# Kernel optimization log

Measured on AMD Instinct MI355X. Metric: run time of the kernel, lower is better.

## Reference

```python
import jax, jax.numpy as jnp
import numpy as np

N = 100000      # nodes
E = 1600000     # edges (before self loops)
F_IN = 256      # num_features
HID = 8         # hid per head, layer 1
H1 = 8          # in_head
H2 = 4          # out_head
NCLS = 40       # num_classes


def setup_inputs() -> dict:
    key = jax.random.key(0)
    ks = jax.random.split(key, 10)
    p = lambda k, shape: jax.random.normal(k, shape, jnp.float32) * 0.1
    d1 = H1 * HID   # 64
    d2 = H2 * NCLS  # 160
    return dict(
        x=jax.random.normal(ks[0], (N, F_IN), jnp.float32),
        edge_index=jax.random.randint(ks[1], (2, E), 0, N),
        Wl1=p(ks[2], (F_IN, d1)), bl1=jnp.zeros((d1,), jnp.float32),
        Wr1=p(ks[3], (F_IN, d1)), br1=jnp.zeros((d1,), jnp.float32),
        att1=p(ks[4], (H1, HID)), b1=jnp.zeros((d1,), jnp.float32),
        Wl2=p(ks[5], (d1, d2)), bl2=jnp.zeros((d2,), jnp.float32),
        Wr2=p(ks[6], (d1, d2)), br2=jnp.zeros((d2,), jnp.float32),
        att2=p(ks[7], (H2, NCLS)), b2=jnp.zeros((NCLS,), jnp.float32),
    )


def gatv2_conv(x, src, dst, Wl, bl, Wr, br, att, bias, heads, ch, concat):
    """PyG GATv2Conv (eval mode): lin_l -> source/messages, lin_r -> target."""
    n = x.shape[0]
    xl = (x @ Wl + bl).reshape(n, heads, ch)   # source-side features
    xr = (x @ Wr + br).reshape(n, heads, ch)   # target-side features
    # edge-wise attention logits: LeakyReLU(x_i + x_j) . att
    e = jax.nn.leaky_relu(xl[src] + xr[dst], 0.2)          # [E, H, C]
    logits = jnp.einsum('ehc,hc->eh', e, att)               # [E, H]
    # segment softmax over incoming edges of each destination node
    m = jax.ops.segment_max(logits, dst, num_segments=n)    # [N, H]
    ex = jnp.exp(logits - m[dst])
    s = jax.ops.segment_sum(ex, dst, num_segments=n)        # [N, H]
    alpha = ex / (s[dst] + 1e-16)                           # [E, H]
    # scatter-add weighted source messages
    out = jax.ops.segment_sum(xl[src] * alpha[:, :, None], dst, num_segments=n)  # [N, H, C]
    if concat:
        return out.reshape(n, heads * ch) + bias
    return out.mean(axis=1) + bias


def reference(x, edge_index, Wl1, bl1, Wr1, br1, att1, b1,
              Wl2, bl2, Wr2, br2, att2, b2):
    n = x.shape[0]
    loop = jnp.arange(n)
    # PyG GATv2Conv default add_self_loops=True
    src = jnp.concatenate([edge_index[0], loop])
    dst = jnp.concatenate([edge_index[1], loop])
    # eval mode: all dropout (input, inter-layer, attention) disabled
    h = gatv2_conv(x, src, dst, Wl1, bl1, Wr1, br1, att1, b1, H1, HID, True)
    h = jax.nn.elu(h)
    out = gatv2_conv(h, src, dst, Wl2, bl2, Wr2, br2, att2, b2, H2, NCLS, False)
    return jax.nn.log_softmax(out, axis=1)
```

## Files before the change

kernel.cpp:

```cpp
#include <hip/hip_runtime.h>
#include <math.h>

#define NN 100000
#define EE 1600000
#define FIN 256
#define D1 64
#define D2 160
#define C2 40
#define PK1 264
#define PK2 72
#define NBUCK 391
#define CAP 5000
#define WSCL 0.015625f
#define L2E 1.442695041f

typedef unsigned short u16;
typedef __attribute__((ext_vector_type(8))) short bf16x8;
typedef __attribute__((ext_vector_type(4))) float f32x4;
typedef _Float16 h2t __attribute__((ext_vector_type(2)));
union hu { unsigned u; h2t h; };

__device__ __forceinline__ u16 f2bf(float f){
  unsigned b = __float_as_uint(f);
  return (u16)((b + 0x7FFFu + ((b >> 16) & 1u)) >> 16);
}
__device__ __forceinline__ u16 f2h(float f){
  union { _Float16 h; u16 u; } c; c.h = (_Float16)f; return c.u;
}
__device__ __forceinline__ float h16f(u16 v){
  union { u16 u; _Float16 h; } c; c.u = v; return (float)c.h;
}

__global__ void wprep_k(const float* __restrict__ Wl1, const float* __restrict__ Wr1,
                        const float* __restrict__ att1,
                        const float* __restrict__ bl1, const float* __restrict__ br1,
                        const float* __restrict__ Wl2, const float* __restrict__ Wr2,
                        const float* __restrict__ att2,
                        const float* __restrict__ bl2, const float* __restrict__ br2,
                        float* __restrict__ WA1, float* __restrict__ BA1,
                        float* __restrict__ WA2, float* __restrict__ BA2){
  int t = blockIdx.x*256 + threadIdx.x;
  if (t < 4096){
    int k = t >> 4, j = t & 15;
    float v = 0.f;
    if (j < 8){
      float s = 0.f;
      #pragma unroll
      for (int c = 0; c < 8; ++c) s += Wl1[(size_t)k*D1 + j*8 + c] * att1[j*8 + c];
      v = 0.6f * s;
    }
    WA1[t] = v;
  } else if (t < 4608){
    int i = t - 4096;
    int k = i >> 3, j = i & 7;
    float v = 0.f;
    if (j < 4){
      float s = 0.f;
      #pragma unroll
      for (int c = 0; c < 40; ++c) s += Wl2[(size_t)k*D2 + j*40 + c] * att2[j*40 + c];
      v = 0.6f * s;
    }
    WA2[i] = v;
  } else if (t < 4616){
    int j = t - 4608;
    float s = 0.f;
    #pragma unroll
    for (int c = 0; c < 8; ++c) s += bl1[j*8 + c] * att1[j*8 + c];
    BA1[j] = 0.6f * s;
  } else if (t < 4620){
    int j = t - 4616;
    float s = 0.f;
    #pragma unroll
    for (int c = 0; c < 40; ++c) s += bl2[j*40 + c] * att2[j*40 + c];
    BA2[j] = 0.6f * s;
  }
}

__global__ __launch_bounds__(256) void part1_k(const int* __restrict__ ei,
                                               int* __restrict__ bcnt,
                                               int* __restrict__ csrtmp){
  __shared__ int hist[NBUCK];
  __shared__ int gbase[NBUCK];
  int t = threadIdx.x;
  for (int i = t; i < NBUCK; i += 256) hist[i] = 0;
  __syncthreads();
  int rb[8], rr[8], rv[8];
  #pragma unroll
  for (int q = 0; q < 8; ++q){
    int e = blockIdx.x*2048 + q*256 + t;
    rb[q] = -1;
    if (e < EE){
      int s = ei[e], d = ei[EE + e];
      int b = d >> 8;
      rb[q] = b;
      rv[q] = s | ((d & 255) << 17);
      rr[q] = atomicAdd(&hist[b], 1);
    }
  }
  __syncthreads();
  for (int i = t; i < NBUCK; i += 256)
    if (hist[i] > 0) gbase[i] = atomicAdd(&bcnt[i], hist[i]);
  __syncthreads();
  #pragma unroll
  for (int q = 0; q < 8; ++q){
    if (rb[q] >= 0){
      int pos = gbase[rb[q]] + rr[q];
      if (pos < CAP) csrtmp[rb[q]*CAP + pos] = rv[q];
    }
  }
}

__global__ __launch_bounds__(256) void sort_k(const int* __restrict__ bcnt,
                                              const int* __restrict__ csrtmp,
                                              int* __restrict__ csr1,
                                              int* __restrict__ csr2,
                                              int* __restrict__ off,
                                              int* __restrict__ end){
  __shared__ int cnt[256];
  __shared__ int sc[256];
  __shared__ int cur[256];
  int b = blockIdx.x, t = threadIdx.x;
  int E = bcnt[b]; if (E > CAP) E = CAP;
  int n = (b << 8) + t;
  cnt[t] = (n < NN) ? 1 : 0;
  __syncthreads();
  for (int i = t; i < E; i += 256){
    int v = csrtmp[b*CAP + i];
    atomicAdd(&cnt[(v >> 17) & 255], 1);
  }
  __syncthreads();
  int x = cnt[t];
  sc[t] = x;
  __syncthreads();
  for (int o = 1; o < 256; o <<= 1){
    int v = (t >= o) ? sc[t - o] : 0;
    __syncthreads();
    sc[t] += v;
    __syncthreads();
  }
  int excl = sc[t] - x;
  if (n < NN){
    off[n] = b*CAP + excl;
    end[n] = b*CAP + excl + x;
    csr1[b*CAP + excl] = n * 128;
    csr2[b*CAP + excl] = n * 8;
    cur[t] = excl + 1;
  } else {
    cur[t] = excl;
  }
  __syncthreads();
  for (int i = t; i < E; i += 256){
    int v = csrtmp[b*CAP + i];
    int p = atomicAdd(&cur[(v >> 17) & 255], 1);
    int src = v & 0x1FFFF;
    csr1[b*CAP + p] = src * 128;
    csr2[b*CAP + p] = src * 8;
  }
}

__global__ __launch_bounds__(256) void gemm1_mfma(
    const float* __restrict__ X,
    const float* __restrict__ Wl, const float* __restrict__ bl,
    const float* __restrict__ Wr, const float* __restrict__ br,
    const float* __restrict__ WA1, const float* __restrict__ BA1,
    u16* __restrict__ outl, u16* __restrict__ outr, u16* __restrict__ w1){
  __shared__ u16 WB[144*PK1];
  int t = threadIdx.x;
  #pragma unroll
  for (int q = 0; q < 16; ++q){
    int idx = t + 256*q;
    int k = idx >> 4, c4 = idx & 15;
    float4 vl = *reinterpret_cast<const float4*>(Wl + (size_t)k*D1 + c4*4);
    float4 vr = *reinterpret_cast<const float4*>(Wr + (size_t)k*D1 + c4*4);
    WB[(c4*4+0)*PK1 + k] = f2bf(vl.x); WB[(c4*4+1)*PK1 + k] = f2bf(vl.y);
    WB[(c4*4+2)*PK1 + k] = f2bf(vl.z); WB[(c4*4+3)*PK1 + k] = f2bf(vl.w);
    WB[(64+c4*4+0)*PK1 + k] = f2bf(vr.x); WB[(64+c4*4+1)*PK1 + k] = f2bf(vr.y);
    WB[(64+c4*4+2)*PK1 + k] = f2bf(vr.z); WB[(64+c4*4+3)*PK1 + k] = f2bf(vr.w);
  }
  #pragma unroll
  for (int q = 0; q < 16; ++q){
    int idx = t + 256*q;
    int k = idx >> 4, j = idx & 15;
    WB[(128+j)*PK1 + k] = f2bf(WA1[k*16 + j]);
  }
  __syncthreads();
  int w = t >> 6, l = t & 63;
  int g = l >> 4;
  int arow = blockIdx.x*64 + w*16 + (l & 15);
  if (arow >= NN) arow = NN-1;
  const float* xp = X + (size_t)arow*FIN + g*8;
  f32x4 acc[9] = {};
  #pragma unroll
  for (int kk = 0; kk < 8; ++kk){
    float4 a0 = *reinterpret_cast<const float4*>(xp + kk*32);
    float4 a1 = *reinterpret_cast<const float4*>(xp + kk*32 + 4);
    union { bf16x8 v; u16 u[8]; } A;
    A.u[0]=f2bf(a0.x); A.u[1]=f2bf(a0.y); A.u[2]=f2bf(a0.z); A.u[3]=f2bf(a0.w);
    A.u[4]=f2bf(a1.x); A.u[5]=f2bf(a1.y); A.u[6]=f2bf(a1.z); A.u[7]=f2bf(a1.w);
    const u16* wb = WB + (l & 15)*PK1 + kk*32 + g*8;
    #pragma unroll
    for (int c = 0; c < 9; ++c){
      bf16x8 B = *reinterpret_cast<const bf16x8*>(wb + c*16*PK1);
      acc[c] = __builtin_amdgcn_mfma_f32_16x16x32_bf16(A.v, B, acc[c], 0, 0, 0);
    }
  }
  int ocol = l & 15;
  int orow0 = blockIdx.x*64 + w*16 + g*4;
  #pragma unroll
  for (int c = 0; c < 8; ++c){
    bool left = (c < 4);
    int col = (left ? c : c-4)*16 + ocol;
    u16* op = left ? outl : outr;
    float bv = (left ? bl : br)[col];
    #pragma unroll
    for (int r = 0; r < 4; ++r){
      int row = orow0 + r;
      if (row < NN) op[(size_t)row*D1 + col] = f2h(acc[c][r] + bv);
    }
  }
  if (ocol < 8){
    float bav = BA1[ocol];
    #pragma unroll
    for (int r = 0; r < 4; ++r){
      int row = orow0 + r;
      if (row < NN) w1[(size_t)row*8 + ocol] = f2h(__expf(acc[8][r] + bav) * WSCL);
    }
  }
}

__global__ __launch_bounds__(256) void gemm2_mfma(
    const u16* __restrict__ H,
    const float* __restrict__ Wl, const float* __restrict__ bl,
    const float* __restrict__ Wr, const float* __restrict__ br,
    const float* __restrict__ WA2, const float* __restrict__ BA2,
    u16* __restrict__ outl, u16* __restrict__ outr, u16* __restrict__ w2){
  __shared__ u16 WB[336*PK2];
  int t = threadIdx.x;
  #pragma unroll
  for (int q = 0; q < 10; ++q){
    int idx = t + 256*q;
    int k = idx / 40, c4 = idx % 40;
    float4 vl = *reinterpret_cast<const float4*>(Wl + (size_t)k*D2 + c4*4);
    float4 vr = *reinterpret_cast<const float4*>(Wr + (size_t)k*D2 + c4*4);
    WB[(c4*4+0)*PK2 + k] = f2bf(vl.x); WB[(c4*4+1)*PK2 + k] = f2bf(vl.y);
    WB[(c4*4+2)*PK2 + k] = f2bf(vl.z); WB[(c4*4+3)*PK2 + k] = f2bf(vl.w);
    WB[(160+c4*4+0)*PK2 + k] = f2bf(vr.x); WB[(160+c4*4+1)*PK2 + k] = f2bf(vr.y);
    WB[(160+c4*4+2)*PK2 + k] = f2bf(vr.z); WB[(160+c4*4+3)*PK2 + k] = f2bf(vr.w);
  }
  #pragma unroll
  for (int q = 0; q < 2; ++q){
    int i2 = t + 256*q;
    int k = i2 >> 3, j = i2 & 7;
    WB[(320+j)*PK2 + k] = f2bf(WA2[k*8 + j]);
    WB[(328+j)*PK2 + k] = 0;
  }
  __syncthreads();
  int w = t >> 6, l = t & 63;
  int g = l >> 4;
  int arow = blockIdx.x*64 + w*16 + (l & 15);
  if (arow >= NN) arow = NN-1;
  const u16* hp = H + (size_t)arow*D1 + g*8;
  f32x4 acc[21] = {};
  #pragma unroll
  for (int kk = 0; kk < 2; ++kk){
    bf16x8 A = *reinterpret_cast<const bf16x8*>(hp + kk*32);
    const u16* wb = WB + (l & 15)*PK2 + kk*32 + g*8;
    #pragma unroll
    for (int c = 0; c < 21; ++c){
      bf16x8 B = *reinterpret_cast<const bf16x8*>(wb + c*16*PK2);
      acc[c] = __builtin_amdgcn_mfma_f32_16x16x32_bf16(A, B, acc[c], 0, 0, 0);
    }
  }
  int ocol = l & 15;
  int orow0 = blockIdx.x*64 + w*16 + g*4;
  #pragma unroll
  for (int c = 0; c < 20; ++c){
    bool left = (c < 10);
    int col = (left ? c : c-10)*16 + ocol;
    u16* op = left ? outl : outr;
    float bv = (left ? bl : br)[col];
    #pragma unroll
    for (int r = 0; r < 4; ++r){
      int row = orow0 + r;
      if (row < NN) op[(size_t)row*D2 + col] = f2h(acc[c][r] + bv);
    }
  }
  if (ocol < 4){
    float bav = BA2[ocol];
    #pragma unroll
    for (int r = 0; r < 4; ++r){
      int row = orow0 + r;
      if (row < NN) w2[(size_t)row*4 + ocol] = f2h(__expf(acc[20][r] + bav) * WSCL);
    }
  }
}

__global__ void l1_fused(const u16* __restrict__ xl, const u16* __restrict__ xr,
                         const u16* __restrict__ w1,
                         const int* __restrict__ off, const int* __restrict__ end,
                         const int* __restrict__ csr1,
                         const float* __restrict__ att,
                         const float* __restrict__ b, u16* __restrict__ out){
  int tid = threadIdx.x;
  int lane = tid & 63;
  int g = (lane >> 4) & 1, l = lane & 15;
  int n = blockIdx.x*8 + (tid >> 6)*2 + (lane >> 5);
  if (n >= NN) return;
  int h = l >> 1;
  const char* xlb = (const char*)xl;
  const char* w1b = (const char*)w1;
  int lo = 8*l;
  int wo = 2*h;
  uint2 xru = *reinterpret_cast<const uint2*>(xr + (size_t)n*D1 + 4*l);
  hu r0, r1; r0.u = xru.x; r1.u = xru.y;
  hu a0, a1;
  a0.h[0] = (_Float16)(0.4f*L2E*att[4*l+0]); a0.h[1] = (_Float16)(0.4f*L2E*att[4*l+1]);
  a1.h[0] = (_Float16)(0.4f*L2E*att[4*l+2]); a1.h[1] = (_Float16)(0.4f*L2E*att[4*l+3]);
  float s = 0.f;
  hu acc0, acc1; acc0.u = 0; acc1.u = 0;
  int p = off[n] + g, e1 = end[n];
  for (; p + 6 < e1; p += 8){
    unsigned bo[4];
    #pragma unroll
    for (int q = 0; q < 4; ++q) bo[q] = (unsigned)csr1[p + 2*q];
    uint2 uv[4]; u16 wv[4];
    #pragma unroll
    for (int q = 0; q < 4; ++q){
      uv[q] = *reinterpret_cast<const uint2*>(xlb + bo[q] + lo);
      wv[q] = *reinterpret_cast<const u16*>(w1b + (bo[q] >> 3) + wo);
    }
    #pragma unroll
    for (int q = 0; q < 4; ++q){
      hu x0, x1; x0.u = uv[q].x; x1.u = uv[q].y;
      hu y0, y1; y0.h = x0.h + r0.h; y1.h = x1.h + r1.h;
      y0.u &= 0x7FFF7FFFu; y1.u &= 0x7FFF7FFFu;
      hu t2; t2.h = a0.h*y0.h + a1.h*y1.h;
      float tf = (float)t2.h[0] + (float)t2.h[1];
      tf += __shfl_xor(tf, 1);
      float pa = __builtin_amdgcn_exp2f(tf) * h16f(wv[q]);
      s += pa;
      hu pp; pp.h[0] = (_Float16)pa; pp.h[1] = pp.h[0];
      acc0.h = pp.h*x0.h + acc0.h;
      acc1.h = pp.h*x1.h + acc1.h;
    }
  }
  for (; p < e1; p += 2){
    unsigned bo = (unsigned)csr1[p];
    uint2 ua = *reinterpret_cast<const uint2*>(xlb + bo + lo);
    u16 wa = *reinterpret_cast<const u16*>(w1b + (bo >> 3) + wo);
    hu x0, x1; x0.u = ua.x; x1.u = ua.y;
    hu y0, y1; y0.h = x0.h + r0.h; y1.h = x1.h + r1.h;
    y0.u &= 0x7FFF7FFFu; y1.u &= 0x7FFF7FFFu;
    hu t2; t2.h = a0.h*y0.h + a1.h*y1.h;
    float tf = (float)t2.h[0] + (float)t2.h[1];
    tf += __shfl_xor(tf, 1);
    float pa = __builtin_amdgcn_exp2f(tf) * h16f(wa);
    s += pa;
    hu pp; pp.h[0] = (_Float16)pa; pp.h[1] = pp.h[0];
    acc0.h = pp.h*x0.h + acc0.h;
    acc1.h = pp.h*x1.h + acc1.h;
  }
  s += __shfl_xor(s, 16);
  { hu m; m.u = (unsigned)__shfl_xor((int)acc0.u, 16); acc0.h = acc0.h + m.h; }
  { hu m; m.u = (unsigned)__shfl_xor((int)acc1.u, 16); acc1.h = acc1.h + m.h; }
  if (g == 0){
    float inv = 1.f / (s + 1e-16f);
    float v0 = (float)acc0.h[0]*inv + b[4*l+0];
    float v1 = (float)acc0.h[1]*inv + b[4*l+1];
    float v2 = (float)acc1.h[0]*inv + b[4*l+2];
    float v3 = (float)acc1.h[1]*inv + b[4*l+3];
    ushort4 o;
    o.x = f2bf(v0 > 0.f ? v0 : expm1f(v0));
    o.y = f2bf(v1 > 0.f ? v1 : expm1f(v1));
    o.z = f2bf(v2 > 0.f ? v2 : expm1f(v2));
    o.w = f2bf(v3 > 0.f ? v3 : expm1f(v3));
    *reinterpret_cast<ushort4*>(out + (size_t)n*D1 + 4*l) = o;
  }
}

__global__ void l2_fused(const u16* __restrict__ xl, const u16* __restrict__ xr,
                         const u16* __restrict__ w2,
                         const int* __restrict__ off, const int* __restrict__ end,
                         const int* __restrict__ csr2,
                         const float* __restrict__ att,
                         const float* __restrict__ b, float* __restrict__ out){
  int tid = threadIdx.x;
  int lane = tid & 63;
  int g = (lane >> 4) & 1, l = lane & 15;
  int n = blockIdx.x*8 + (tid >> 6)*2 + (lane >> 5);
  if (n >= NN) return;
  int h = l >> 2;
  int c0 = 10*l;
  const char* xlb = (const char*)xl;
  const char* w2b = (const char*)w2;
  int lo = 20*l;
  int wo = 2*h;
  hu xr2[5], a2[5];
  #pragma unroll
  for (int d = 0; d < 5; ++d){
    xr2[d].u = *reinterpret_cast<const unsigned*>(xr + (size_t)n*D2 + c0 + 2*d);
    a2[d].h[0] = (_Float16)(0.4f*L2E*att[c0 + 2*d]);
    a2[d].h[1] = (_Float16)(0.4f*L2E*att[c0 + 2*d + 1]);
  }
  float s = 0.f;
  hu acc2[5];
  #pragma unroll
  for (int d = 0; d < 5; ++d) acc2[d].u = 0;
  int p = off[n] + g, e1 = end[n];
  for (; p + 6 < e1; p += 8){
    unsigned b8[4];
    #pragma unroll
    for (int q = 0; q < 4; ++q) b8[q] = (unsigned)csr2[p + 2*q];
    hu xa[4][5]; u16 wv[4];
    #pragma unroll
    for (int q = 0; q < 4; ++q){
      const char* rp = xlb + b8[q]*40u + lo;
      #pragma unroll
      for (int d = 0; d < 5; ++d) xa[q][d].u = *reinterpret_cast<const unsigned*>(rp + 4*d);
      wv[q] = *reinterpret_cast<const u16*>(w2b + b8[q] + wo);
    }
    #pragma unroll
    for (int q = 0; q < 4; ++q){
      hu t2; t2.u = 0;
      #pragma unroll
      for (int d = 0; d < 5; ++d){
        hu y; y.h = xa[q][d].h + xr2[d].h; y.u &= 0x7FFF7FFFu;
        t2.h = a2[d].h*y.h + t2.h;
      }
      float tf = (float)t2.h[0] + (float)t2.h[1];
      tf += __shfl_xor(tf, 1); tf += __shfl_xor(tf, 2);
      float pa = __builtin_amdgcn_exp2f(tf) * h16f(wv[q]);
      s += pa;
      hu pp; pp.h[0] = (_Float16)pa; pp.h[1] = pp.h[0];
      #pragma unroll
      for (int d = 0; d < 5; ++d) acc2[d].h = pp.h*xa[q][d].h + acc2[d].h;
    }
  }
  for (; p < e1; p += 2){
    unsigned b8 = (unsigned)csr2[p];
    const char* rp = xlb + b8*40u + lo;
    hu xa[5];
    #pragma unroll
    for (int d = 0; d < 5; ++d) xa[d].u = *reinterpret_cast<const unsigned*>(rp + 4*d);
    u16 wa16 = *reinterpret_cast<const u16*>(w2b + b8 + wo);
    hu ta2; ta2.u = 0;
    #pragma unroll
    for (int d = 0; d < 5; ++d){
      hu ya; ya.h = xa[d].h + xr2[d].h; ya.u &= 0x7FFF7FFFu;
      ta2.h = a2[d].h*ya.h + ta2.h;
    }
    float ta = (float)ta2.h[0] + (float)ta2.h[1];
    ta += __shfl_xor(ta, 1); ta += __shfl_xor(ta, 2);
    float pa = __builtin_amdgcn_exp2f(ta) * h16f(wa16);
    s += pa;
    hu ppa; ppa.h[0] = (_Float16)pa; ppa.h[1] = ppa.h[0];
    #pragma unroll
    for (int d = 0; d < 5; ++d) acc2[d].h = ppa.h*xa[d].h + acc2[d].h;
  }
  s += __shfl_xor(s, 16);
  #pragma unroll
  for (int d = 0; d < 5; ++d){
    hu m; m.u = (unsigned)__shfl_xor((int)acc2[d].u, 16);
    acc2[d].h = acc2[d].h + m.h;
  }
  float inv = 1.f / (s + 1e-16f);
  float v[10];
  #pragma unroll
  for (int d = 0; d < 5; ++d){
    v[2*d]   = (float)acc2[d].h[0] * inv;
    v[2*d+1] = (float)acc2[d].h[1] * inv;
  }
  #pragma unroll
  for (int k = 0; k < 10; ++k){
    float o = v[k];
    o += __shfl_xor(o, 4);
    o += __shfl_xor(o, 8);
    v[k] = o*0.25f + b[10*(l & 3) + k];
  }
  float mx = v[0];
  #pragma unroll
  for (int k = 1; k < 10; ++k) mx = fmaxf(mx, v[k]);
  mx = fmaxf(mx, __shfl_xor(mx, 1));
  mx = fmaxf(mx, __shfl_xor(mx, 2));
  float es = 0.f;
  #pragma unroll
  for (int k = 0; k < 10; ++k) es += __expf(v[k] - mx);
  es += __shfl_xor(es, 1);
  es += __shfl_xor(es, 2);
  float lse = mx + __logf(es);
  if (g == 0 && l < 4){
    float* op = out + (size_t)n*C2 + 10*l;
    #pragma unroll
    for (int k2 = 0; k2 < 5; ++k2)
      *reinterpret_cast<float2*>(op + 2*k2) = make_float2(v[2*k2] - lse, v[2*k2+1] - lse);
  }
}

extern "C" void kernel_launch(void* const* d_in, const int* in_sizes, int n_in,
                              void* d_out, int out_size, void* d_ws, size_t ws_size,
                              hipStream_t stream){
  const float* x    = (const float*)d_in[0];
  const int*   ei   = (const int*)  d_in[1];
  const float* Wl1  = (const float*)d_in[2];
  const float* bl1  = (const float*)d_in[3];
  const float* Wr1  = (const float*)d_in[4];
  const float* br1  = (const float*)d_in[5];
  const float* att1 = (const float*)d_in[6];
  const float* b1   = (const float*)d_in[7];
  const float* Wl2  = (const float*)d_in[8];
  const float* bl2  = (const float*)d_in[9];
  const float* Wr2  = (const float*)d_in[10];
  const float* br2  = (const float*)d_in[11];
  const float* att2 = (const float*)d_in[12];
  const float* b2   = (const float*)d_in[13];
  float* out = (float*)d_out;

  char* ws = (char*)d_ws;
  u16*   B1     = (u16*)  (ws);
  u16*   B2     = (u16*)  (ws + 13000000);
  u16*   W1     = (u16*)  (ws + 26000000);
  u16*   h1     = (u16*)  (ws + 28000000);
  u16*   B3     = (u16*)  (ws + 41000000);
  u16*   W2     = (u16*)  (ws + 73500000);
  u16*   B4     = (u16*)  (ws + 74500000);
  int*   csrtmp = (int*)  (ws + 74500000);
  float* WA1    = (float*)(ws + 107000000);
  float* BA1    = (float*)(ws + 107100000);
  float* WA2    = (float*)(ws + 107200000);
  float* BA2    = (float*)(ws + 107300000);
  int*   off    = (int*)  (ws + 107400000);
  int*   end    = (int*)  (ws + 107900000);
  int*   bcnt   = (int*)  (ws + 108400000);
  int*   csr1   = (int*)  (ws + 108500000);
  int*   csr2   = (int*)  (ws + 116400000);
  const int blk = 256;
  const int MB = (NN + 63)/64;

  hipMemsetAsync(bcnt, 0, (size_t)NBUCK*4, stream);
  part1_k<<<(EE + 2047)/2048, blk, 0, stream>>>(ei, bcnt, csrtmp);
  sort_k <<<NBUCK, blk, 0, stream>>>(bcnt, csrtmp, csr1, csr2, off, end);
  wprep_k<<<19, blk, 0, stream>>>(Wl1, Wr1, att1, bl1, br1,
                                  Wl2, Wr2, att2, bl2, br2, WA1, BA1, WA2, BA2);

  gemm1_mfma<<<MB, blk, 0, stream>>>(x, Wl1, bl1, Wr1, br1, WA1, BA1, B1, B2, W1);
  l1_fused  <<<(NN + 7)/8, blk, 0, stream>>>(B1, B2, W1, off, end, csr1, att1, b1, h1);

  gemm2_mfma<<<MB, blk, 0, stream>>>(h1, Wl2, bl2, Wr2, br2, WA2, BA2, B3, B4, W2);
  l2_fused  <<<(NN + 7)/8, blk, 0, stream>>>(B3, B4, W2, off, end, csr2, att2, b2, out);
}
```

Baseline: 339.2 us.

## Merge CSR arrays into one index array and remap layer-1 aggregation to one node per wave

The sort kernel now writes a single CSR array of src*16 instead of two scaled copies, which halves CSR write and read traffic, and both layer kernels derive their byte offsets from it. Layer-1 aggregation now gives each 64-lane wave one node: 8 lanes each own one head and load 16 bytes, and 8 edge groups are processed in parallel. This drops the per-edge intra-head shuffle and the unrolled 4-edge batching in exchange for a 3-step cross-group shuffle reduction and less memory-level parallelism per lane. More lanes may sit idle on low-degree nodes.

```diff
diff --git a/kernel.cpp b/kernel.cpp
--- a/kernel.cpp
+++ b/kernel.cpp
@@ -112,8 +112,7 @@
 
 __global__ __launch_bounds__(256) void sort_k(const int* __restrict__ bcnt,
                                               const int* __restrict__ csrtmp,
-                                              int* __restrict__ csr1,
-                                              int* __restrict__ csr2,
+                                              int* __restrict__ csrm,
                                               int* __restrict__ off,
                                               int* __restrict__ end){
   __shared__ int cnt[256];
@@ -142,8 +141,7 @@
   if (n < NN){
     off[n] = b*CAP + excl;
     end[n] = b*CAP + excl + x;
-    csr1[b*CAP + excl] = n * 128;
-    csr2[b*CAP + excl] = n * 8;
+    csrm[b*CAP + excl] = n * 16;
     cur[t] = excl + 1;
   } else {
     cur[t] = excl;
@@ -152,9 +150,7 @@
   for (int i = t; i < E; i += 256){
     int v = csrtmp[b*CAP + i];
     int p = atomicAdd(&cur[(v >> 17) & 255], 1);
-    int src = v & 0x1FFFF;
-    csr1[b*CAP + p] = src * 128;
-    csr2[b*CAP + p] = src * 8;
+    csrm[b*CAP + p] = (v & 0x1FFFF) * 16;
   }
 }
 
@@ -298,90 +294,86 @@
 __global__ void l1_fused(const u16* __restrict__ xl, const u16* __restrict__ xr,
                          const u16* __restrict__ w1,
                          const int* __restrict__ off, const int* __restrict__ end,
-                         const int* __restrict__ csr1,
+                         const int* __restrict__ csrm,
                          const float* __restrict__ att,
                          const float* __restrict__ b, u16* __restrict__ out){
   int tid = threadIdx.x;
   int lane = tid & 63;
-  int g = (lane >> 4) & 1, l = lane & 15;
-  int n = blockIdx.x*8 + (tid >> 6)*2 + (lane >> 5);
+  int g = lane >> 3, l = lane & 7;
+  int n = blockIdx.x*4 + (tid >> 6);
   if (n >= NN) return;
-  int h = l >> 1;
   const char* xlb = (const char*)xl;
   const char* w1b = (const char*)w1;
-  int lo = 8*l;
-  int wo = 2*h;
-  uint2 xru = *reinterpret_cast<const uint2*>(xr + (size_t)n*D1 + 4*l);
-  hu r0, r1; r0.u = xru.x; r1.u = xru.y;
-  hu a0, a1;
-  a0.h[0] = (_Float16)(0.4f*L2E*att[4*l+0]); a0.h[1] = (_Float16)(0.4f*L2E*att[4*l+1]);
-  a1.h[0] = (_Float16)(0.4f*L2E*att[4*l+2]); a1.h[1] = (_Float16)(0.4f*L2E*att[4*l+3]);
+  int lo = 16*l;
+  int wo = 2*l;
+  uint4 xru = *reinterpret_cast<const uint4*>(xr + (size_t)n*D1 + 8*l);
+  hu r0, r1, r2, r3; r0.u = xru.x; r1.u = xru.y; r2.u = xru.z; r3.u = xru.w;
+  hu a0, a1, a2, a3;
+  a0.h[0] = (_Float16)(0.4f*L2E*att[8*l+0]); a0.h[1] = (_Float16)(0.4f*L2E*att[8*l+1]);
+  a1.h[0] = (_Float16)(0.4f*L2E*att[8*l+2]); a1.h[1] = (_Float16)(0.4f*L2E*att[8*l+3]);
+  a2.h[0] = (_Float16)(0.4f*L2E*att[8*l+4]); a2.h[1] = (_Float16)(0.4f*L2E*att[8*l+5]);
+  a3.h[0] = (_Float16)(0.4f*L2E*att[8*l+6]); a3.h[1] = (_Float16)(0.4f*L2E*att[8*l+7]);
   float s = 0.f;
-  hu acc0, acc1; acc0.u = 0; acc1.u = 0;
+  hu acc0, acc1, acc2, acc3; acc0.u = acc1.u = acc2.u = acc3.u = 0;
   int p = off[n] + g, e1 = end[n];
-  for (; p + 6 < e1; p += 8){
-    unsigned bo[4];
-    #pragma unroll
-    for (int q = 0; q < 4; ++q) bo[q] = (unsigned)csr1[p + 2*q];
-    uint2 uv[4]; u16 wv[4];
-    #pragma unroll
-    for (int q = 0; q < 4; ++q){
-      uv[q] = *reinterpret_cast<const uint2*>(xlb + bo[q] + lo);
-      wv[q] = *reinterpret_cast<const u16*>(w1b + (bo[q] >> 3) + wo);
-    }
-    #pragma unroll
-    for (int q = 0; q < 4; ++q){
-      hu x0, x1; x0.u = uv[q].x; x1.u = uv[q].y;
-      hu y0, y1; y0.h = x0.h + r0.h; y1.h = x1.h + r1.h;
-      y0.u &= 0x7FFF7FFFu; y1.u &= 0x7FFF7FFFu;
-      hu t2; t2.h = a0.h*y0.h + a1.h*y1.h;
-      float tf = (float)t2.h[0] + (float)t2.h[1];
-      tf += __shfl_xor(tf, 1);
-      float pa = __builtin_amdgcn_exp2f(tf) * h16f(wv[q]);
-      s += pa;
-      hu pp; pp.h[0] = (_Float16)pa; pp.h[1] = pp.h[0];
-      acc0.h = pp.h*x0.h + acc0.h;
-      acc1.h = pp.h*x1.h + acc1.h;
-    }
-  }
-  for (; p < e1; p += 2){
-    unsigned bo = (unsigned)csr1[p];
-    uint2 ua = *reinterpret_cast<const uint2*>(xlb + bo + lo);
-    u16 wa = *reinterpret_cast<const u16*>(w1b + (bo >> 3) + wo);
-    hu x0, x1; x0.u = ua.x; x1.u = ua.y;
-    hu y0, y1; y0.h = x0.h + r0.h; y1.h = x1.h + r1.h;
+  for (; p < e1; p += 8){
+    unsigned v = (unsigned)csrm[p];
+    uint4 ua = *reinterpret_cast<const uint4*>(xlb + (v << 3) + lo);
+    u16 wa = *reinterpret_cast<const u16*>(w1b + v + wo);
+    hu x0, x1, x2, x3; x0.u = ua.x; x1.u = ua.y; x2.u = ua.z; x3.u = ua.w;
+    hu y0, y1, y2, y3;
+    y0.h = x0.h + r0.h; y1.h = x1.h + r1.h;
+    y2.h = x2.h + r2.h; y3.h = x3.h + r3.h;
     y0.u &= 0x7FFF7FFFu; y1.u &= 0x7FFF7FFFu;
+    y2.u &= 0x7FFF7FFFu; y3.u &= 0x7FFF7FFFu;
     hu t2; t2.h = a0.h*y0.h + a1.h*y1.h;
+    t2.h = a2.h*y2.h + t2.h;
+    t2.h = a3.h*y3.h + t2.h;
     float tf = (float)t2.h[0] + (float)t2.h[1];
-    tf += __shfl_xor(tf, 1);
     float pa = __builtin_amdgcn_exp2f(tf) * h16f(wa);
     s += pa;
     hu pp; pp.h[0] = (_Float16)pa; pp.h[1] = pp.h[0];
     acc0.h = pp.h*x0.h + acc0.h;
     acc1.h = pp.h*x1.h + acc1.h;
-  }
-  s += __shfl_xor(s, 16);
-  { hu m; m.u = (unsigned)__shfl_xor((int)acc0.u, 16); acc0.h = acc0.h + m.h; }
-  { hu m; m.u = (unsigned)__shfl_xor((int)acc1.u, 16); acc1.h = acc1.h + m.h; }
+    acc2.h = pp.h*x2.h + acc2.h;
+    acc3.h = pp.h*x3.h + acc3.h;
+  }
+  #pragma unroll
+  for (int d = 8; d <= 32; d <<= 1){
+    s += __shfl_xor(s, d);
+    { hu m; m.u = (unsigned)__shfl_xor((int)acc0.u, d); acc0.h = acc0.h + m.h; }
+    { hu m; m.u = (unsigned)__shfl_xor((int)acc1.u, d); acc1.h = acc1.h + m.h; }
+    { hu m; m.u = (unsigned)__shfl_xor((int)acc2.u, d); acc2.h = acc2.h + m.h; }
+    { hu m; m.u = (unsigned)__shfl_xor((int)acc3.u, d); acc3.h = acc3.h + m.h; }
+  }
   if (g == 0){
     float inv = 1.f / (s + 1e-16f);
-    float v0 = (float)acc0.h[0]*inv + b[4*l+0];
-    float v1 = (float)acc0.h[1]*inv + b[4*l+1];
-    float v2 = (float)acc1.h[0]*inv + b[4*l+2];
-    float v3 = (float)acc1.h[1]*inv + b[4*l+3];
-    ushort4 o;
-    o.x = f2bf(v0 > 0.f ? v0 : expm1f(v0));
-    o.y = f2bf(v1 > 0.f ? v1 : expm1f(v1));
-    o.z = f2bf(v2 > 0.f ? v2 : expm1f(v2));
-    o.w = f2bf(v3 > 0.f ? v3 : expm1f(v3));
-    *reinterpret_cast<ushort4*>(out + (size_t)n*D1 + 4*l) = o;
+    float v0 = (float)acc0.h[0]*inv + b[8*l+0];
+    float v1 = (float)acc0.h[1]*inv + b[8*l+1];
+    float v2 = (float)acc1.h[0]*inv + b[8*l+2];
+    float v3 = (float)acc1.h[1]*inv + b[8*l+3];
+    float v4 = (float)acc2.h[0]*inv + b[8*l+4];
+    float v5 = (float)acc2.h[1]*inv + b[8*l+5];
+    float v6 = (float)acc3.h[0]*inv + b[8*l+6];
+    float v7 = (float)acc3.h[1]*inv + b[8*l+7];
+    ushort4 o0, o1;
+    o0.x = f2bf(v0 > 0.f ? v0 : expm1f(v0));
+    o0.y = f2bf(v1 > 0.f ? v1 : expm1f(v1));
+    o0.z = f2bf(v2 > 0.f ? v2 : expm1f(v2));
+    o0.w = f2bf(v3 > 0.f ? v3 : expm1f(v3));
+    o1.x = f2bf(v4 > 0.f ? v4 : expm1f(v4));
+    o1.y = f2bf(v5 > 0.f ? v5 : expm1f(v5));
+    o1.z = f2bf(v6 > 0.f ? v6 : expm1f(v6));
+    o1.w = f2bf(v7 > 0.f ? v7 : expm1f(v7));
+    *reinterpret_cast<ushort4*>(out + (size_t)n*D1 + 8*l)     = o0;
+    *reinterpret_cast<ushort4*>(out + (size_t)n*D1 + 8*l + 4) = o1;
   }
 }
 
 __global__ void l2_fused(const u16* __restrict__ xl, const u16* __restrict__ xr,
                          const u16* __restrict__ w2,
                          const int* __restrict__ off, const int* __restrict__ end,
-                         const int* __restrict__ csr2,
+                         const int* __restrict__ csrm,
                          const float* __restrict__ att,
                          const float* __restrict__ b, float* __restrict__ out){
   int tid = threadIdx.x;
@@ -408,16 +400,16 @@
   for (int d = 0; d < 5; ++d) acc2[d].u = 0;
   int p = off[n] + g, e1 = end[n];
   for (; p + 6 < e1; p += 8){
-    unsigned b8[4];
-    #pragma unroll
-    for (int q = 0; q < 4; ++q) b8[q] = (unsigned)csr2[p + 2*q];
+    unsigned bv[4];
+    #pragma unroll
+    for (int q = 0; q < 4; ++q) bv[q] = (unsigned)csrm[p + 2*q];
     hu xa[4][5]; u16 wv[4];
     #pragma unroll
     for (int q = 0; q < 4; ++q){
-      const char* rp = xlb + b8[q]*40u + lo;
+      const char* rp = xlb + bv[q]*20u + lo;
       #pragma unroll
       for (int d = 0; d < 5; ++d) xa[q][d].u = *reinterpret_cast<const unsigned*>(rp + 4*d);
-      wv[q] = *reinterpret_cast<const u16*>(w2b + b8[q] + wo);
+      wv[q] = *reinterpret_cast<const u16*>(w2b + (bv[q] >> 1) + wo);
     }
     #pragma unroll
     for (int q = 0; q < 4; ++q){
@@ -437,12 +429,12 @@
     }
   }
   for (; p < e1; p += 2){
-    unsigned b8 = (unsigned)csr2[p];
-    const char* rp = xlb + b8*40u + lo;
+    unsigned bv = (unsigned)csrm[p];
+    const char* rp = xlb + bv*20u + lo;
     hu xa[5];
     #pragma unroll
     for (int d = 0; d < 5; ++d) xa[d].u = *reinterpret_cast<const unsigned*>(rp + 4*d);
-    u16 wa16 = *reinterpret_cast<const u16*>(w2b + b8 + wo);
+    u16 wa16 = *reinterpret_cast<const u16*>(w2b + (bv >> 1) + wo);
     hu ta2; ta2.u = 0;
     #pragma unroll
     for (int d = 0; d < 5; ++d){
@@ -531,20 +523,19 @@
   int*   off    = (int*)  (ws + 107400000);
   int*   end    = (int*)  (ws + 107900000);
   int*   bcnt   = (int*)  (ws + 108400000);
-  int*   csr1   = (int*)  (ws + 108500000);
-  int*   csr2   = (int*)  (ws + 116400000);
+  int*   csrm   = (int*)  (ws + 108500000);
   const int blk = 256;
   const int MB = (NN + 63)/64;
 
   hipMemsetAsync(bcnt, 0, (size_t)NBUCK*4, stream);
   part1_k<<<(EE + 2047)/2048, blk, 0, stream>>>(ei, bcnt, csrtmp);
-  sort_k <<<NBUCK, blk, 0, stream>>>(bcnt, csrtmp, csr1, csr2, off, end);
+  sort_k <<<NBUCK, blk, 0, stream>>>(bcnt, csrtmp, csrm, off, end);
   wprep_k<<<19, blk, 0, stream>>>(Wl1, Wr1, att1, bl1, br1,
                                   Wl2, Wr2, att2, bl2, br2, WA1, BA1, WA2, BA2);
 
   gemm1_mfma<<<MB, blk, 0, stream>>>(x, Wl1, bl1, Wr1, br1, WA1, BA1, B1, B2, W1);
-  l1_fused  <<<(NN + 7)/8, blk, 0, stream>>>(B1, B2, W1, off, end, csr1, att1, b1, h1);
+  l1_fused  <<<(NN + 3)/4, blk, 0, stream>>>(B1, B2, W1, off, end, csrm, att1, b1, h1);
 
   gemm2_mfma<<<MB, blk, 0, stream>>>(h1, Wl2, bl2, Wr2, br2, WA2, BA2, B3, B4, W2);
-  l2_fused  <<<(NN + 7)/8, blk, 0, stream>>>(B3, B4, W2, off, end, csr2, att2, b2, out);
-}
+  l2_fused  <<<(NN + 7)/8, blk, 0, stream>>>(B3, B4, W2, off, end, csrm, att2, b2, out);
+}
```

After: 351.3 us. 1.04x slower.
